# Kernel tuning notes

Hardware: AMD Instinct MI355X
Metric: run time of the kernel (lower is better)

The kernel has to match this reference:

```python
import jax, jax.numpy as jnp
import numpy as np

B = 256          # batch
IMG = 28         # img_width
K = 9            # kernel_size
NUM_CLASSES = 10
NUM_ITER = 3
NUM_ROUTE = 32 * 6 * 6  # 1152


def _conv(x, w, b, stride):
    # x: [B,C,H,W], w: [O,I,K,K] (OIHW), VALID padding as in nn.Conv2d(padding=0)
    y = jax.lax.conv_general_dilated(x, w, (stride, stride), 'VALID',
                                     dimension_numbers=('NCHW', 'OIHW', 'NCHW'))
    return y + b[None, :, None, None]


def _squash(t, axis=-1):
    sq = jnp.sum(t * t, axis=axis, keepdims=True)
    return (sq / (1.0 + sq)) * t / jnp.sqrt(sq)


def setup_inputs() -> dict:
    key = jax.random.key(0)
    ks = jax.random.split(key, 10)
    rn = lambda k, s, sc=0.05: jax.random.normal(k, s, dtype=jnp.float32) * sc
    return {
        'x': jax.random.uniform(ks[0], (B, 1, IMG, IMG), dtype=jnp.float32),
        'conv1_w': rn(ks[1], (256, 1, K, K)),
        'conv1_b': jnp.zeros((256,), jnp.float32),
        # 8 primary-capsule convs of 32 channels stacked as one 256-out conv
        'prim_w': rn(ks[2], (8 * 32, 256, K, K)),
        'prim_b': jnp.zeros((8 * 32,), jnp.float32),
        # torch.randn init, std 1, shape [num_capsules, num_route_nodes, in, out]
        'route_w': jax.random.normal(ks[3], (NUM_CLASSES, NUM_ROUTE, 8, 16), dtype=jnp.float32),
        'dec_w1': rn(ks[4], (16 * NUM_CLASSES, 512)),
        'dec_b1': jnp.zeros((512,), jnp.float32),
        'dec_w2': rn(ks[5], (512, 1024)),
        'dec_b2': jnp.zeros((1024,), jnp.float32),
        'dec_w3': rn(ks[6], (1024, IMG * IMG)),
        'dec_b3': jnp.zeros((IMG * IMG,), jnp.float32),
    }


def reference(x, conv1_w, conv1_b, prim_w, prim_b, route_w,
              dec_w1, dec_b1, dec_w2, dec_b2, dec_w3, dec_b3):
    b = x.shape[0]
    # conv1 + relu: [B,256,20,20]
    h = jax.nn.relu(_conv(x, conv1_w, conv1_b, 1))
    # primary capsules: [B,8*32,6,6] -> [B,1152,8] (capsule c flattens its own 32x6x6 block)
    p = _conv(h, prim_w, prim_b, 2)
    p = p.reshape(b, 8, -1).transpose(0, 2, 1)
    p = _squash(p)  # squash over the 8-dim capsule vectors
    # priors: [10,B,1152,1,16]
    priors = jnp.einsum('bri,crio->cbro', p, route_w)[:, :, :, None, :]
    logits = jnp.zeros_like(priors)
    outputs = None
    for i in range(NUM_ITER):
        probs = jax.nn.softmax(logits, axis=2)            # over route nodes
        outputs = _squash(jnp.sum(probs * priors, axis=2, keepdims=True))  # [10,B,1,1,16]
        if i != NUM_ITER - 1:
            logits = logits + jnp.sum(priors * outputs, axis=-1, keepdims=True)
    v = outputs.reshape(NUM_CLASSES, b, 16).transpose(1, 0, 2)  # [B,10,16]
    classes = jax.nn.softmax(jnp.sqrt(jnp.sum(v * v, axis=-1)), axis=1)  # [B,10]
    # y is None path: one-hot of argmax class
    y = jax.nn.one_hot(jnp.argmax(classes, axis=1), NUM_CLASSES, dtype=v.dtype)
    masked = (v * y[:, :, None]).reshape(b, -1)  # [B,160]
    h1 = jax.nn.relu(masked @ dec_w1 + dec_b1)
    h2 = jax.nn.relu(h1 @ dec_w2 + dec_b2)
    recon = jax.nn.sigmoid(h2 @ dec_w3 + dec_b3)  # [B,784]
    return classes, recon
```

## Files before the change

### kernel.cpp

```cpp
#include <hip/hip_runtime.h>
#include <hip/hip_bf16.h>
#include <math.h>

constexpr int BB = 256;
constexpr int NCLS = 10;
constexpr int NROUTE = 1152;

typedef __attribute__((ext_vector_type(8))) short s16x8;
typedef __attribute__((ext_vector_type(4))) float f32x4;

__global__ __launch_bounds__(256) void k_conv1b(const float* __restrict__ x,
    const float* __restrict__ w, const float* __restrict__ bias,
    __hip_bfloat16* __restrict__ hT_hi, __hip_bfloat16* __restrict__ hT_lo,
    int b0) {
  int b_l = blockIdx.x >> 2, q = blockIdx.x & 3;
  __shared__ float sx[784];
  __shared__ float sw[64 * 81];
  int t = threadIdx.x;
  for (int i = t; i < 784; i += 256) sx[i] = x[(size_t)(b0 + b_l) * 784 + i];
  for (int i = t; i < 5184; i += 256) sw[i] = w[(size_t)q * 5184 + i];
  __syncthreads();
  int oc = q * 64 + (t & 63);
  int wv = t >> 6;
  float wreg[81];
#pragma unroll
  for (int k = 0; k < 81; ++k) wreg[k] = sw[(t & 63) * 81 + k];
  float bv = bias[oc];
  for (int st = wv * 10; st < wv * 10 + 10; ++st) {
    int y = st >> 1, x0 = (st & 1) * 10;
    float acc[10];
#pragma unroll
    for (int i = 0; i < 10; ++i) acc[i] = bv;
#pragma unroll
    for (int ky = 0; ky < 9; ++ky) {
      const float* row = &sx[(y + ky) * 28 + x0];
      float rv[18];
#pragma unroll
      for (int i = 0; i < 18; ++i) rv[i] = row[i];
#pragma unroll
      for (int kx = 0; kx < 9; ++kx) {
        float wgt = wreg[ky * 9 + kx];
#pragma unroll
        for (int xi = 0; xi < 10; ++xi) acc[xi] = fmaf(rv[kx + xi], wgt, acc[xi]);
      }
    }
#pragma unroll
    for (int xi = 0; xi < 10; ++xi) {
      float av = fmaxf(acc[xi], 0.f);
      __hip_bfloat16 hi = __float2bfloat16(av);
      float lo = av - __bfloat162float(hi);
      size_t idx = ((size_t)(b_l * 400 + y * 20 + x0 + xi)) * 256 + oc;
      hT_hi[idx] = hi;
      hT_lo[idx] = __float2bfloat16(lo);
    }
  }
}

__global__ __launch_bounds__(256) void k_cvtw(const float* __restrict__ w,
    __hip_bfloat16* __restrict__ wt_hi, __hip_bfloat16* __restrict__ wt_lo) {
  int oc = blockIdx.x >> 2, icq = blockIdx.x & 3;
  __shared__ float sw[5184];
  int t = threadIdx.x;
  const float* src = w + ((size_t)oc * 256 + icq * 64) * 81;
  for (int i = t; i < 5184; i += 256) sw[i] = src[i];
  __syncthreads();
  for (int i = t; i < 5184; i += 256) {
    int tap = i >> 6, icl = i & 63;
    float v = sw[icl * 81 + tap];
    __hip_bfloat16 hi = __float2bfloat16(v);
    float lo = v - __bfloat162float(hi);
    size_t dst = (size_t)tap * 65536 + (size_t)oc * 256 + icq * 64 + icl;
    wt_hi[dst] = hi;
    wt_lo[dst] = __float2bfloat16(lo);
  }
}

constexpr int P6_BUF = 32768;

__global__ __launch_bounds__(512, 2) void k_prim6(
    const __hip_bfloat16* __restrict__ hT_hi, const __hip_bfloat16* __restrict__ hT_lo,
    const __hip_bfloat16* __restrict__ wt_hi, const __hip_bfloat16* __restrict__ wt_lo,
    float* __restrict__ pout) {
  __shared__ __align__(16) char lds[2 * P6_BUF];
  int x = blockIdx.x & 7, g = blockIdx.x >> 3;
  int nM = (x < 4) ? 5 : 4;
  if (g >= nM * 6) return;
  int Mblk = x + (g / 6) * 8;
  int rem = g % 6;
  int kb = rem % 3, Nblk = rem / 3;
  int m0 = Mblk * 128, oc0 = Nblk * 128;
  int t = threadIdx.x, wv = t >> 6, lane = t & 63;
  int jswz = (t & 3) ^ ((t >> 2) & 3);
  int rA = t >> 2;
  size_t roA;
  {
    int m = m0 + rA;
    int b = m / 36, s = m - b * 36, oy = s / 6, ox = s - oy * 6;
    roA = ((size_t)(b * 400 + oy * 40 + ox * 2)) * 512 + (size_t)(jswz * 16);
  }
  size_t boB = ((size_t)(oc0 + rA)) * 512 + (size_t)(jswz * 16);
  const char* hTh = (const char*)hT_hi;
  const char* hTl = (const char*)hT_lo;
  const char* wth = (const char*)wt_hi;
  const char* wtl = (const char*)wt_lo;

  int4 rah, ral, rbh, rbl;
  auto loadregs = [&](int s) {
    int tt = s >> 3, icc = s & 7;
    int tap = kb * 27 + tt;
    int ky = tap / 9, kx = tap - ky * 9;
    size_t offA = (size_t)((ky * 20 + kx) * 512 + icc * 64);
    size_t offB = (size_t)tap * 131072 + (size_t)(icc * 64);
    rah = *(const int4*)(hTh + roA + offA);
    ral = *(const int4*)(hTl + roA + offA);
    rbh = *(const int4*)(wth + boB + offB);
    rbl = *(const int4*)(wtl + boB + offB);
  };
  auto writeregs = [&](int bufi) {
    char* d = lds + bufi * P6_BUF + t * 16;
    *(int4*)(d) = rah;
    *(int4*)(d + 8192) = ral;
    *(int4*)(d + 16384) = rbh;
    *(int4*)(d + 24576) = rbl;
  };

  int wr = wv >> 2, wc = wv & 3;
  int lr = lane & 15;
  int swz16 = ((lane >> 4) ^ (lane & 3)) * 16;
  int arow[4], brow[2];
#pragma unroll
  for (int i = 0; i < 4; ++i) arow[i] = (wr * 64 + i * 16 + lr) * 64 + swz16;
#pragma unroll
  for (int j = 0; j < 2; ++j) brow[j] = 16384 + (wc * 32 + j * 16 + lr) * 64 + swz16;

  f32x4 acc[4][2];
#pragma unroll
  for (int i = 0; i < 4; ++i)
#pragma unroll
    for (int j = 0; j < 2; ++j) acc[i][j] = (f32x4){0.f, 0.f, 0.f, 0.f};

  loadregs(0);
  writeregs(0);
  __syncthreads();

#pragma unroll 1
  for (int s = 0; s < 216; ++s) {
    int cur = s & 1;
    if (s < 215) loadregs(s + 1);
    const char* Ab = lds + cur * P6_BUF;
    s16x8 ah[4], al[4], bh[2], bl[2];
#pragma unroll
    for (int i = 0; i < 4; ++i) {
      ah[i] = *(const s16x8*)(Ab + arow[i]);
      al[i] = *(const s16x8*)(Ab + 8192 + arow[i]);
    }
#pragma unroll
    for (int j = 0; j < 2; ++j) {
      bh[j] = *(const s16x8*)(Ab + brow[j]);
      bl[j] = *(const s16x8*)(Ab + 8192 + brow[j]);
    }
#pragma unroll
    for (int i = 0; i < 4; ++i)
#pragma unroll
      for (int j = 0; j < 2; ++j) {
        acc[i][j] = __builtin_amdgcn_mfma_f32_16x16x32_bf16(ah[i], bh[j], acc[i][j], 0, 0, 0);
        acc[i][j] = __builtin_amdgcn_mfma_f32_16x16x32_bf16(ah[i], bl[j], acc[i][j], 0, 0, 0);
        acc[i][j] = __builtin_amdgcn_mfma_f32_16x16x32_bf16(al[i], bh[j], acc[i][j], 0, 0, 0);
      }
    if (s < 215) writeregs(cur ^ 1);
    __syncthreads();
  }
  float* pb = pout + (size_t)kb * (4608 * 256);
#pragma unroll
  for (int i = 0; i < 4; ++i)
#pragma unroll
    for (int j = 0; j < 2; ++j) {
      int n = oc0 + wc * 32 + j * 16 + lr;
#pragma unroll
      for (int qq = 0; qq < 4; ++qq) {
        int m = m0 + wr * 64 + i * 16 + (lane >> 4) * 4 + qq;
        pb[(size_t)m * 256 + n] = acc[i][j][qq];
      }
    }
}

__global__ __launch_bounds__(256) void k_squash3(const float* __restrict__ pout,
    const float* __restrict__ bias, float* __restrict__ psT, int b0) {
  int s = blockIdx.x;
  int b_l = blockIdx.y;
  int t = threadIdx.x;
  int c32 = t & 31;
  __shared__ float ws[4][32];
  __shared__ float buf2[256];
  size_t base = ((size_t)(b_l * 36 + s)) * 256 + t;
  float val = pout[base] + pout[base + 1179648] + pout[base + 2359296] + bias[t];
  float v2 = val * val;
  v2 += __shfl_xor(v2, 32);
  int wvv = t >> 6, lane = t & 63;
  if (lane < 32) ws[wvv][lane] = v2;
  __syncthreads();
  float ss = ws[0][c32] + ws[1][c32] + ws[2][c32] + ws[3][c32];
  float sc = sqrtf(ss) / (1.f + ss);
  buf2[t] = val * sc;
  __syncthreads();
  int cc = t >> 3, jj = t & 7;
  psT[(size_t)(b0 + b_l) * 9216 + (size_t)cc * 288 + s * 8 + jj] =
      buf2[jj * 32 + cc];
}

__global__ __launch_bounds__(768) void k_route5(const float* __restrict__ psT,
    const float* __restrict__ rw, float* __restrict__ vout) {
  int c = blockIdx.x >> 8;
  int b = blockIdx.x & 255;
  int tid = threadIdx.x;
  int wave = tid >> 6, lane = tid & 63;
  int oh = lane >> 5;
  int rs = wave * 32 + (lane & 31);
  __shared__ float lredm[12];
  __shared__ float lreds[12];
  __shared__ float ored[12][2][8];
  __shared__ float osum[16];
  __shared__ float vsq[16];

  float pri[3][8];
  float lgr[3] = {0.f, 0.f, 0.f};
#pragma unroll
  for (int k = 0; k < 3; ++k)
#pragma unroll
    for (int j = 0; j < 8; ++j) pri[k][j] = 0.f;

#pragma unroll
  for (int k = 0; k < 3; ++k) {
    int r = rs + k * 384;
    const float* wr_ = &rw[((size_t)c * 1152 + r) * 128 + oh * 8];
    const float4* pp = (const float4*)&psT[((size_t)b * 1152 + r) * 8];
    float4 pa = pp[0], pb4 = pp[1];
    float ps8[8] = {pa.x, pa.y, pa.z, pa.w, pb4.x, pb4.y, pb4.z, pb4.w};
#pragma unroll
    for (int i = 0; i < 8; ++i) {
      float4 w0 = *(const float4*)&wr_[i * 16];
      float4 w1 = *(const float4*)&wr_[i * 16 + 4];
      float w8[8] = {w0.x, w0.y, w0.z, w0.w, w1.x, w1.y, w1.z, w1.w};
#pragma unroll
      for (int j = 0; j < 8; ++j) pri[k][j] = fmaf(ps8[i], w8[j], pri[k][j]);
    }
  }

  for (int it = 0; it < 3; ++it) {
    float a[8];
    if (it == 0) {
      const float invu = 1.f / 1152.f;
#pragma unroll
      for (int j = 0; j < 8; ++j)
        a[j] = (pri[0][j] + pri[1][j] + pri[2][j]) * invu;
    } else {
      float mx = fmaxf(fmaxf(lgr[0], lgr[1]), lgr[2]);
#pragma unroll
      for (int off = 16; off; off >>= 1) mx = fmaxf(mx, __shfl_xor(mx, off));
      if (lane == 0) lredm[wave] = mx;
      __syncthreads();
      mx = lredm[0];
      for (int w = 1; w < 12; ++w) mx = fmaxf(mx, lredm[w]);
      float er[3];
      float sm = 0.f;
#pragma unroll
      for (int k = 0; k < 3; ++k) {
        er[k] = expf(lgr[k] - mx);
        sm += er[k];
      }
#pragma unroll
      for (int off = 16; off; off >>= 1) sm += __shfl_xor(sm, off);
      if (lane == 0) lreds[wave] = sm;
      __syncthreads();
      float s = 0.f;
      for (int w = 0; w < 12; ++w) s += lreds[w];
      float inv = 1.f / s;
#pragma unroll
      for (int j = 0; j < 8; ++j) a[j] = 0.f;
#pragma unroll
      for (int k = 0; k < 3; ++k) {
        float p = er[k] * inv;
#pragma unroll
        for (int j = 0; j < 8; ++j) a[j] = fmaf(p, pri[k][j], a[j]);
      }
    }
#pragma unroll
    for (int off = 16; off; off >>= 1)
#pragma unroll
      for (int j = 0; j < 8; ++j) a[j] += __shfl_xor(a[j], off);
    if ((lane & 31) == 0) {
#pragma unroll
      for (int j = 0; j < 8; ++j) ored[wave][oh][j] = a[j];
    }
    __syncthreads();
    if (tid < 16) {
      float s = 0.f;
      for (int w = 0; w < 12; ++w) s += ored[w][tid >> 3][tid & 7];
      osum[tid] = s;
    }
    __syncthreads();
    if (tid < 16) {
      float sqv = 0.f;
#pragma unroll
      for (int o = 0; o < 16; ++o) sqv += osum[o] * osum[o];
      float sc = sqrtf(sqv) / (1.f + sqv);
      vsq[tid] = osum[tid] * sc;
    }
    __syncthreads();
    if (it < 2) {
      float vh[8];
#pragma unroll
      for (int j = 0; j < 8; ++j) vh[j] = vsq[oh * 8 + j];
#pragma unroll
      for (int k = 0; k < 3; ++k) {
        float d = 0.f;
#pragma unroll
        for (int j = 0; j < 8; ++j) d = fmaf(pri[k][j], vh[j], d);
        d += __shfl_xor(d, 32);
        lgr[k] += d;
      }
      __syncthreads();
    }
  }
  if (tid < 16) vout[((size_t)c * BB + b) * 16 + tid] = vsq[tid];
}

__global__ __launch_bounds__(64) void k_cls2(const float* __restrict__ v,
                                             float* __restrict__ classes,
                                             int* __restrict__ am,
                                             float* __restrict__ vsel) {
  int b = blockIdx.x;
  int t = threadIdx.x;
  __shared__ float snrm[10];
  __shared__ int samax;
  if (t < 10) {
    float sq = 0.f;
#pragma unroll
    for (int o = 0; o < 16; ++o) {
      float xx = v[(size_t)(t * BB + b) * 16 + o];
      sq += xx * xx;
    }
    snrm[t] = sqrtf(sq);
  }
  __syncthreads();
  if (t == 0) {
    int amx = 0;
    float bm = snrm[0];
    for (int cc = 1; cc < 10; ++cc)
      if (snrm[cc] > bm) { bm = snrm[cc]; amx = cc; }
    samax = amx;
    am[b] = amx;
  }
  __syncthreads();
  if (t < 10) {
    float mx = snrm[0];
    for (int cc = 1; cc < 10; ++cc) mx = fmaxf(mx, snrm[cc]);
    float sm = 0.f;
    for (int cc = 0; cc < 10; ++cc) sm += expf(snrm[cc] - mx);
    classes[b * 10 + t] = expf(snrm[t] - mx) / sm;
  }
  if (t < 16) vsel[b * 16 + t] = v[((size_t)samax * BB + b) * 16 + t];
}

__global__ __launch_bounds__(512) void k_fc1s(const float* __restrict__ vsel,
    const int* __restrict__ am, const float* __restrict__ w1,
    const float* __restrict__ b1, float* __restrict__ h1) {
  int b = blockIdx.x;
  int n = threadIdx.x;
  __shared__ float sv[16];
  __shared__ int sam;
  if (n < 16) sv[n] = vsel[b * 16 + n];
  if (n == 0) sam = am[b];
  __syncthreads();
  float acc = b1[n];
  int base = sam * 16;
#pragma unroll
  for (int i = 0; i < 16; ++i)
    acc = fmaf(sv[i], w1[(size_t)(base + i) * 512 + n], acc);
  h1[(size_t)b * 512 + n] = fmaxf(acc, 0.f);
}

template <int ACT>
__global__ __launch_bounds__(256) void k_fc32(const float* __restrict__ A,
                                              const float* __restrict__ W,
                                              const float* __restrict__ bias,
                                              float* __restrict__ O, int M,
                                              int N, int K) {
  int n0 = blockIdx.x * 32, m0 = blockIdx.y * 32;
  __shared__ float sa[32][33];
  __shared__ float sb[32][34];
  int tid = threadIdx.x, ty = tid >> 4, tx = tid & 15;
  float acc[2][2] = {};
  for (int k0 = 0; k0 < K; k0 += 32) {
    __syncthreads();
    for (int i = tid; i < 1024; i += 256) {
      int m = i >> 5, k = i & 31;
      sa[m][k] = A[(size_t)(m0 + m) * K + k0 + k];
      int kk = i >> 5, n = i & 31;
      int nn = n0 + n;
      sb[kk][n] = (nn < N) ? W[(size_t)(k0 + kk) * N + nn] : 0.f;
    }
    __syncthreads();
#pragma unroll
    for (int k = 0; k < 32; ++k) {
      float a0 = sa[ty * 2 + 0][k];
      float a1 = sa[ty * 2 + 1][k];
      float b0 = sb[k][tx * 2 + 0];
      float b1v = sb[k][tx * 2 + 1];
      acc[0][0] = fmaf(a0, b0, acc[0][0]);
      acc[0][1] = fmaf(a0, b1v, acc[0][1]);
      acc[1][0] = fmaf(a1, b0, acc[1][0]);
      acc[1][1] = fmaf(a1, b1v, acc[1][1]);
    }
  }
#pragma unroll
  for (int i = 0; i < 2; ++i) {
    int m = m0 + ty * 2 + i;
#pragma unroll
    for (int j = 0; j < 2; ++j) {
      int n = n0 + tx * 2 + j;
      if (n < N) {
        float xv = acc[i][j] + bias[n];
        if (ACT == 0)
          xv = fmaxf(xv, 0.f);
        else
          xv = 1.f / (1.f + expf(-xv));
        O[(size_t)m * N + n] = xv;
      }
    }
  }
}

extern "C" void kernel_launch(void* const* d_in, const int* in_sizes, int n_in,
                              void* d_out, int out_size, void* d_ws,
                              size_t ws_size, hipStream_t stream) {
  (void)in_sizes; (void)n_in; (void)out_size; (void)ws_size;
  const float* x       = (const float*)d_in[0];
  const float* conv1_w = (const float*)d_in[1];
  const float* conv1_b = (const float*)d_in[2];
  const float* prim_w  = (const float*)d_in[3];
  const float* prim_b  = (const float*)d_in[4];
  const float* route_w = (const float*)d_in[5];
  const float* dec_w1  = (const float*)d_in[6];
  const float* dec_b1  = (const float*)d_in[7];
  const float* dec_w2  = (const float*)d_in[8];
  const float* dec_b2  = (const float*)d_in[9];
  const float* dec_w3  = (const float*)d_in[10];
  const float* dec_b3  = (const float*)d_in[11];
  float* out = (float*)d_out;

  char* wsb = (char*)d_ws;
  __hip_bfloat16* hT_hi = (__hip_bfloat16*)(wsb);
  __hip_bfloat16* hT_lo = (__hip_bfloat16*)(wsb + 26214400);
  __hip_bfloat16* wt_hi = (__hip_bfloat16*)(wsb + 52428800);
  __hip_bfloat16* wt_lo = (__hip_bfloat16*)(wsb + 63045632);
  float* pout = (float*)(wsb + 73662464);
  float* psT  = (float*)(wsb + 87818240);
  float* v    = (float*)(wsb + 97255424);
  float* h1   = (float*)(wsb + 97419264);
  float* h2   = (float*)(wsb + 97943552);
  int*   am   = (int*)  (wsb + 98992128);
  float* vsel = (float*)(wsb + 98996224);

  k_cvtw<<<1024, 256, 0, stream>>>(prim_w, wt_hi, wt_lo);
  for (int hh = 0; hh < 2; ++hh) {
    int b0 = hh * 128;
    k_conv1b<<<512, 256, 0, stream>>>(x, conv1_w, conv1_b, hT_hi, hT_lo, b0);
    k_prim6<<<240, 512, 0, stream>>>(hT_hi, hT_lo, wt_hi, wt_lo, pout);
    k_squash3<<<dim3(36, 128), 256, 0, stream>>>(pout, prim_b, psT, b0);
  }
  k_route5<<<2560, 768, 0, stream>>>(psT, route_w, v);
  k_cls2<<<256, 64, 0, stream>>>(v, out, am, vsel);
  k_fc1s<<<256, 512, 0, stream>>>(vsel, am, dec_w1, dec_b1, h1);
  k_fc32<0><<<dim3(32, 8), 256, 0, stream>>>(h1, dec_w2, dec_b2, h2, 256, 1024, 512);
  k_fc32<1><<<dim3(25, 8), 256, 0, stream>>>(h2, dec_w3, dec_b3, out + 2560, 256, 784, 1024);
}
```

Before: 769.9 us.

## Process two batch items per routing block and fuse class head with fc1

The routing kernel now handles two batch items per block, so each route_w load is reused across both items and the grid is halved. Each thread covers six route nodes and four output dims instead of three and eight. The softmax over route nodes drops the max subtraction and uses fast __expf, removing one cross-wave reduction and barrier per iteration at some risk of overflow. The class softmax/argmax kernel and the fc1 kernel are merged into one launch, which eliminates the intermediate am/vsel buffers.

```diff
diff --git a/kernel.cpp b/kernel.cpp
--- a/kernel.cpp
+++ b/kernel.cpp
@@ -208,131 +208,153 @@
       buf2[jj * 32 + cc];
 }
 
-__global__ __launch_bounds__(768) void k_route5(const float* __restrict__ psT,
+__global__ __launch_bounds__(768) void k_route6(const float* __restrict__ psT,
     const float* __restrict__ rw, float* __restrict__ vout) {
-  int c = blockIdx.x >> 8;
-  int b = blockIdx.x & 255;
+  int c = blockIdx.x >> 7;
+  int bp = blockIdx.x & 127;
+  int b0 = bp * 2;
   int tid = threadIdx.x;
   int wave = tid >> 6, lane = tid & 63;
-  int oh = lane >> 5;
-  int rs = wave * 32 + (lane & 31);
-  __shared__ float lredm[12];
-  __shared__ float lreds[12];
-  __shared__ float ored[12][2][8];
-  __shared__ float osum[16];
-  __shared__ float vsq[16];
-
-  float pri[3][8];
-  float lgr[3] = {0.f, 0.f, 0.f};
-#pragma unroll
-  for (int k = 0; k < 3; ++k)
-#pragma unroll
-    for (int j = 0; j < 8; ++j) pri[k][j] = 0.f;
-
-#pragma unroll
-  for (int k = 0; k < 3; ++k) {
-    int r = rs + k * 384;
-    const float* wr_ = &rw[((size_t)c * 1152 + r) * 128 + oh * 8];
-    const float4* pp = (const float4*)&psT[((size_t)b * 1152 + r) * 8];
-    float4 pa = pp[0], pb4 = pp[1];
-    float ps8[8] = {pa.x, pa.y, pa.z, pa.w, pb4.x, pb4.y, pb4.z, pb4.w};
+  int rl = lane & 15;
+  int oq = lane >> 4;
+  int rs = wave * 16 + rl;
+  __shared__ float lreds[12][2];
+  __shared__ float ored[12][4][2][4];
+  __shared__ float vsq[2][16];
+
+  float pri[2][6][4];
+  float lgr[2][6];
+#pragma unroll
+  for (int b = 0; b < 2; ++b)
+#pragma unroll
+    for (int k = 0; k < 6; ++k) {
+      lgr[b][k] = 0.f;
+#pragma unroll
+      for (int j = 0; j < 4; ++j) pri[b][k][j] = 0.f;
+    }
+
+  for (int k = 0; k < 6; ++k) {
+    int r = rs + k * 192;
+    const float* wr_ = &rw[((size_t)c * 1152 + r) * 128 + oq * 4];
+    const float4* pp = (const float4*)&psT[((size_t)b0 * 1152 + r) * 8];
+    const float4* pq = (const float4*)&psT[((size_t)(b0 + 1) * 1152 + r) * 8];
+    float4 pa0 = pp[0], pa1 = pp[1], pb0 = pq[0], pb1 = pq[1];
+    float psa[8] = {pa0.x, pa0.y, pa0.z, pa0.w, pa1.x, pa1.y, pa1.z, pa1.w};
+    float psb[8] = {pb0.x, pb0.y, pb0.z, pb0.w, pb1.x, pb1.y, pb1.z, pb1.w};
 #pragma unroll
     for (int i = 0; i < 8; ++i) {
-      float4 w0 = *(const float4*)&wr_[i * 16];
-      float4 w1 = *(const float4*)&wr_[i * 16 + 4];
-      float w8[8] = {w0.x, w0.y, w0.z, w0.w, w1.x, w1.y, w1.z, w1.w};
-#pragma unroll
-      for (int j = 0; j < 8; ++j) pri[k][j] = fmaf(ps8[i], w8[j], pri[k][j]);
+      float4 w4 = *(const float4*)&wr_[i * 16];
+      float wa[4] = {w4.x, w4.y, w4.z, w4.w};
+#pragma unroll
+      for (int j = 0; j < 4; ++j) {
+        pri[0][k][j] = fmaf(psa[i], wa[j], pri[0][k][j]);
+        pri[1][k][j] = fmaf(psb[i], wa[j], pri[1][k][j]);
+      }
     }
   }
 
   for (int it = 0; it < 3; ++it) {
-    float a[8];
+    float a[2][4];
     if (it == 0) {
       const float invu = 1.f / 1152.f;
 #pragma unroll
-      for (int j = 0; j < 8; ++j)
-        a[j] = (pri[0][j] + pri[1][j] + pri[2][j]) * invu;
+      for (int b = 0; b < 2; ++b)
+#pragma unroll
+        for (int j = 0; j < 4; ++j) {
+          float s = 0.f;
+#pragma unroll
+          for (int k = 0; k < 6; ++k) s += pri[b][k][j];
+          a[b][j] = s * invu;
+        }
     } else {
-      float mx = fmaxf(fmaxf(lgr[0], lgr[1]), lgr[2]);
-#pragma unroll
-      for (int off = 16; off; off >>= 1) mx = fmaxf(mx, __shfl_xor(mx, off));
-      if (lane == 0) lredm[wave] = mx;
+      float sm[2] = {0.f, 0.f};
+#pragma unroll
+      for (int b = 0; b < 2; ++b)
+#pragma unroll
+        for (int k = 0; k < 6; ++k) sm[b] += __expf(lgr[b][k]);
+#pragma unroll
+      for (int off = 1; off < 16; off <<= 1)
+#pragma unroll
+        for (int b = 0; b < 2; ++b) sm[b] += __shfl_xor(sm[b], off);
+      if (lane == 0) { lreds[wave][0] = sm[0]; lreds[wave][1] = sm[1]; }
       __syncthreads();
-      mx = lredm[0];
-      for (int w = 1; w < 12; ++w) mx = fmaxf(mx, lredm[w]);
-      float er[3];
-      float sm = 0.f;
-#pragma unroll
-      for (int k = 0; k < 3; ++k) {
-        er[k] = expf(lgr[k] - mx);
-        sm += er[k];
-      }
-#pragma unroll
-      for (int off = 16; off; off >>= 1) sm += __shfl_xor(sm, off);
-      if (lane == 0) lreds[wave] = sm;
-      __syncthreads();
+      float inv[2];
+#pragma unroll
+      for (int b = 0; b < 2; ++b) {
+        float s = 0.f;
+        for (int w = 0; w < 12; ++w) s += lreds[w][b];
+        inv[b] = 1.f / s;
+      }
+#pragma unroll
+      for (int b = 0; b < 2; ++b)
+#pragma unroll
+        for (int j = 0; j < 4; ++j) a[b][j] = 0.f;
+#pragma unroll
+      for (int k = 0; k < 6; ++k)
+#pragma unroll
+        for (int b = 0; b < 2; ++b) {
+          float p = __expf(lgr[b][k]) * inv[b];
+#pragma unroll
+          for (int j = 0; j < 4; ++j) a[b][j] = fmaf(p, pri[b][k][j], a[b][j]);
+        }
+    }
+#pragma unroll
+    for (int off = 1; off < 16; off <<= 1)
+#pragma unroll
+      for (int b = 0; b < 2; ++b)
+#pragma unroll
+        for (int j = 0; j < 4; ++j) a[b][j] += __shfl_xor(a[b][j], off);
+    if (rl == 0) {
+#pragma unroll
+      for (int b = 0; b < 2; ++b)
+#pragma unroll
+        for (int j = 0; j < 4; ++j) ored[wave][oq][b][j] = a[b][j];
+    }
+    __syncthreads();
+    if (tid < 32) {
+      int b = tid >> 4, o = tid & 15;
       float s = 0.f;
-      for (int w = 0; w < 12; ++w) s += lreds[w];
-      float inv = 1.f / s;
-#pragma unroll
-      for (int j = 0; j < 8; ++j) a[j] = 0.f;
-#pragma unroll
-      for (int k = 0; k < 3; ++k) {
-        float p = er[k] * inv;
-#pragma unroll
-        for (int j = 0; j < 8; ++j) a[j] = fmaf(p, pri[k][j], a[j]);
-      }
-    }
-#pragma unroll
-    for (int off = 16; off; off >>= 1)
-#pragma unroll
-      for (int j = 0; j < 8; ++j) a[j] += __shfl_xor(a[j], off);
-    if ((lane & 31) == 0) {
-#pragma unroll
-      for (int j = 0; j < 8; ++j) ored[wave][oh][j] = a[j];
-    }
-    __syncthreads();
-    if (tid < 16) {
-      float s = 0.f;
-      for (int w = 0; w < 12; ++w) s += ored[w][tid >> 3][tid & 7];
-      osum[tid] = s;
-    }
-    __syncthreads();
-    if (tid < 16) {
-      float sqv = 0.f;
-#pragma unroll
-      for (int o = 0; o < 16; ++o) sqv += osum[o] * osum[o];
-      float sc = sqrtf(sqv) / (1.f + sqv);
-      vsq[tid] = osum[tid] * sc;
+      for (int w = 0; w < 12; ++w) s += ored[w][o >> 2][b][o & 3];
+      float s2 = s * s;
+#pragma unroll
+      for (int off = 1; off < 16; off <<= 1) s2 += __shfl_xor(s2, off);
+      float sc = sqrtf(s2) / (1.f + s2);
+      vsq[b][o] = s * sc;
     }
     __syncthreads();
     if (it < 2) {
-      float vh[8];
-#pragma unroll
-      for (int j = 0; j < 8; ++j) vh[j] = vsq[oh * 8 + j];
-#pragma unroll
-      for (int k = 0; k < 3; ++k) {
-        float d = 0.f;
-#pragma unroll
-        for (int j = 0; j < 8; ++j) d = fmaf(pri[k][j], vh[j], d);
-        d += __shfl_xor(d, 32);
-        lgr[k] += d;
+#pragma unroll
+      for (int b = 0; b < 2; ++b) {
+        float vh[4];
+#pragma unroll
+        for (int j = 0; j < 4; ++j) vh[j] = vsq[b][oq * 4 + j];
+#pragma unroll
+        for (int k = 0; k < 6; ++k) {
+          float d = 0.f;
+#pragma unroll
+          for (int j = 0; j < 4; ++j) d = fmaf(pri[b][k][j], vh[j], d);
+          d += __shfl_xor(d, 16);
+          d += __shfl_xor(d, 32);
+          lgr[b][k] += d;
+        }
       }
       __syncthreads();
     }
   }
-  if (tid < 16) vout[((size_t)c * BB + b) * 16 + tid] = vsq[tid];
-}
-
-__global__ __launch_bounds__(64) void k_cls2(const float* __restrict__ v,
-                                             float* __restrict__ classes,
-                                             int* __restrict__ am,
-                                             float* __restrict__ vsel) {
+  if (tid < 32) {
+    int b = tid >> 4, o = tid & 15;
+    vout[((size_t)c * BB + (b0 + b)) * 16 + o] = vsq[b][o];
+  }
+}
+
+__global__ __launch_bounds__(512) void k_head(const float* __restrict__ v,
+    const float* __restrict__ w1, const float* __restrict__ b1,
+    float* __restrict__ classes, float* __restrict__ h1) {
   int b = blockIdx.x;
   int t = threadIdx.x;
   __shared__ float snrm[10];
-  __shared__ int samax;
+  __shared__ float sv[16];
+  __shared__ int sam;
   if (t < 10) {
     float sq = 0.f;
 #pragma unroll
@@ -348,36 +370,24 @@
     float bm = snrm[0];
     for (int cc = 1; cc < 10; ++cc)
       if (snrm[cc] > bm) { bm = snrm[cc]; amx = cc; }
-    samax = amx;
-    am[b] = amx;
+    sam = amx;
   }
   __syncthreads();
   if (t < 10) {
     float mx = snrm[0];
     for (int cc = 1; cc < 10; ++cc) mx = fmaxf(mx, snrm[cc]);
-    float sm = 0.f;
-    for (int cc = 0; cc < 10; ++cc) sm += expf(snrm[cc] - mx);
-    classes[b * 10 + t] = expf(snrm[t] - mx) / sm;
-  }
-  if (t < 16) vsel[b * 16 + t] = v[((size_t)samax * BB + b) * 16 + t];
-}
-
-__global__ __launch_bounds__(512) void k_fc1s(const float* __restrict__ vsel,
-    const int* __restrict__ am, const float* __restrict__ w1,
-    const float* __restrict__ b1, float* __restrict__ h1) {
-  int b = blockIdx.x;
-  int n = threadIdx.x;
-  __shared__ float sv[16];
-  __shared__ int sam;
-  if (n < 16) sv[n] = vsel[b * 16 + n];
-  if (n == 0) sam = am[b];
-  __syncthreads();
-  float acc = b1[n];
+    float smv = 0.f;
+    for (int cc = 0; cc < 10; ++cc) smv += __expf(snrm[cc] - mx);
+    classes[b * 10 + t] = __expf(snrm[t] - mx) / smv;
+  }
+  if (t < 16) sv[t] = v[((size_t)sam * BB + b) * 16 + t];
+  __syncthreads();
+  float acc = b1[t];
   int base = sam * 16;
 #pragma unroll
   for (int i = 0; i < 16; ++i)
-    acc = fmaf(sv[i], w1[(size_t)(base + i) * 512 + n], acc);
-  h1[(size_t)b * 512 + n] = fmaxf(acc, 0.f);
+    acc = fmaf(sv[i], w1[(size_t)(base + i) * 512 + t], acc);
+  h1[(size_t)b * 512 + t] = fmaxf(acc, 0.f);
 }
 
 template <int ACT>
@@ -459,8 +469,6 @@
   float* v    = (float*)(wsb + 97255424);
   float* h1   = (float*)(wsb + 97419264);
   float* h2   = (float*)(wsb + 97943552);
-  int*   am   = (int*)  (wsb + 98992128);
-  float* vsel = (float*)(wsb + 98996224);
 
   k_cvtw<<<1024, 256, 0, stream>>>(prim_w, wt_hi, wt_lo);
   for (int hh = 0; hh < 2; ++hh) {
@@ -469,9 +477,8 @@
     k_prim6<<<240, 512, 0, stream>>>(hT_hi, hT_lo, wt_hi, wt_lo, pout);
     k_squash3<<<dim3(36, 128), 256, 0, stream>>>(pout, prim_b, psT, b0);
   }
-  k_route5<<<2560, 768, 0, stream>>>(psT, route_w, v);
-  k_cls2<<<256, 64, 0, stream>>>(v, out, am, vsel);
-  k_fc1s<<<256, 512, 0, stream>>>(vsel, am, dec_w1, dec_b1, h1);
+  k_route6<<<1280, 768, 0, stream>>>(psT, route_w, v);
+  k_head<<<256, 512, 0, stream>>>(v, dec_w1, dec_b1, out, h1);
   k_fc32<0><<<dim3(32, 8), 256, 0, stream>>>(h1, dec_w2, dec_b2, h2, 256, 1024, 512);
   k_fc32<1><<<dim3(25, 8), 256, 0, stream>>>(h2, dec_w3, dec_b3, out + 2560, 256, 784, 1024);
 }
```

Result: faster. 722.8 us (-6.1%).
